# Kernel tuning notes

Hardware: AMD Instinct MI355X
Metric: run time of the kernel (lower is better)

The kernel has to match this reference:

```python
import jax, jax.numpy as jnp
import numpy as np

D_MODEL = 2048
EXPAND = 2
D_INNER = EXPAND * D_MODEL   # 4096
D_STATE = 128
D_CONV = 4
HEADDIM = 64
NHEADS = D_INNER // HEADDIM  # 64
NGROUPS = 1
CONV_DIM = D_INNER + 2 * NGROUPS * D_STATE           # 4352
D_IN_PROJ = 2 * D_INNER + 2 * NGROUPS * D_STATE + NHEADS  # 8512
B, T = 2, 2048
EPS = 1e-5


def setup_inputs() -> dict:
    key = jax.random.key(0)
    ks = jax.random.split(key, 12)
    x = jax.random.normal(ks[0], (B, T, D_MODEL), dtype=jnp.float32)
    cos = jax.random.normal(ks[1], (T, HEADDIM), dtype=jnp.float32)
    sin = jax.random.normal(ks[2], (T, HEADDIM), dtype=jnp.float32)
    in_proj_w = jax.random.normal(ks[3], (D_IN_PROJ, D_MODEL), dtype=jnp.float32) * 0.02
    conv_w = jax.random.normal(ks[4], (CONV_DIM, D_CONV), dtype=jnp.float32) * 0.2
    conv_b = jnp.zeros((CONV_DIM,), dtype=jnp.float32)
    # dt_bias = softplus^{-1}(dt) for dt ~ U[0.001, 0.1]
    dt = jax.random.uniform(ks[5], (NHEADS,), minval=0.001, maxval=0.1)
    dt_bias = (jnp.log(jnp.expm1(dt))).astype(jnp.float32)
    A_log = jnp.log(jax.random.uniform(ks[6], (NHEADS,), minval=1.0, maxval=16.0)).astype(jnp.float32)
    Dskip = jnp.ones((NHEADS,), dtype=jnp.float32)
    norm_w = jnp.ones((D_INNER,), dtype=jnp.float32)
    out_proj_w = jax.random.normal(ks[7], (D_MODEL, D_INNER), dtype=jnp.float32) * 0.02
    return {"x": x, "cos": cos, "sin": sin, "in_proj_w": in_proj_w,
            "conv_w": conv_w, "conv_b": conv_b, "dt_bias": dt_bias,
            "A_log": A_log, "Dskip": Dskip, "norm_w": norm_w,
            "out_proj_w": out_proj_w}


def _mamba2_fwd(x, in_proj_w, conv_w, conv_b, dt_bias, A_log, Dskip, norm_w, out_proj_w):
    # in_proj -> [z, xBC, dt]
    zxbcdt = jnp.einsum('btd,ed->bte', x, in_proj_w)  # [B,T,8512]
    z = zxbcdt[..., :D_INNER]
    xBC = zxbcdt[..., D_INNER:D_INNER + CONV_DIM]
    dt_raw = zxbcdt[..., D_INNER + CONV_DIM:]          # [B,T,H]

    # depthwise causal conv1d + SiLU
    xBC_pad = jnp.pad(xBC, ((0, 0), (D_CONV - 1, 0), (0, 0)))
    conv = conv_b
    for k in range(D_CONV):
        conv = conv + xBC_pad[:, k:k + T, :] * conv_w[:, k]
    xBC = jax.nn.silu(conv)

    x_ssm = xBC[..., :D_INNER].reshape(x.shape[0], T, NHEADS, HEADDIM)  # [B,T,H,P]
    Bmat = xBC[..., D_INNER:D_INNER + D_STATE]                          # [B,T,N] (ngroups=1)
    Cmat = xBC[..., D_INNER + D_STATE:]                                 # [B,T,N]

    dt = jax.nn.softplus(dt_raw + dt_bias)   # [B,T,H]
    A = -jnp.exp(A_log)                      # [H]
    dA = jnp.exp(dt * A)                     # [B,T,H], in (0,1]
    dtx = dt[..., None] * x_ssm              # [B,T,H,P]

    # selective scan over time (state h: [B,H,P,N])
    def step(h, xs_t):
        dA_t, dtx_t, B_t, C_t = xs_t  # [B,H],[B,H,P],[B,N],[B,N]
        h = h * dA_t[:, :, None, None] + dtx_t[:, :, :, None] * B_t[:, None, None, :]
        y = jnp.einsum('bhpn,bn->bhp', h, C_t)
        return h, y

    h0 = jnp.zeros((x.shape[0], NHEADS, HEADDIM, D_STATE), dtype=x.dtype)
    xs = (jnp.swapaxes(dA, 0, 1), jnp.swapaxes(dtx, 0, 1),
          jnp.swapaxes(Bmat, 0, 1), jnp.swapaxes(Cmat, 0, 1))
    _, ys = jax.lax.scan(step, h0, xs)       # ys: [T,B,H,P]
    y = jnp.swapaxes(ys, 0, 1) + Dskip[None, None, :, None] * x_ssm  # [B,T,H,P]
    y = y.reshape(x.shape[0], T, D_INNER)

    # gated RMSNorm: gate first, then normalize
    y = y * jax.nn.silu(z)
    y = y * jax.lax.rsqrt(jnp.mean(jnp.square(y), axis=-1, keepdims=True) + EPS) * norm_w

    return jnp.einsum('bte,de->btd', y, out_proj_w)  # [B,T,D]


def reference(x, cos, sin, in_proj_w, conv_w, conv_b, dt_bias, A_log, Dskip, norm_w, out_proj_w):
    # cos/sin accepted but ignored (Mamba needs no positional encoding)
    return _mamba2_fwd(x, in_proj_w, conv_w, conv_b, dt_bias, A_log, Dskip, norm_w, out_proj_w)
```

## Files before the change

kernel.cpp:

```cpp
#include <hip/hip_runtime.h>

#define D_MODEL 2048
#define D_INNER 4096
#define D_STATE 128
#define HEADDIM 64
#define NHEADS 64
#define CONV_DIM 4352
#define D_IN_PROJ 8512
#define BB 2
#define TSEQ 2048
#define BT (BB*TSEQ)
#define NCHUNK 32
#define LCH 64
#define EPS_F 1e-5f

typedef __bf16 bf16x8 __attribute__((ext_vector_type(8)));
typedef float f32x4 __attribute__((ext_vector_type(4)));

__device__ __forceinline__ float bf2f(unsigned short u){
  unsigned int x = ((unsigned int)u) << 16;
  return __builtin_bit_cast(float, x);
}
__device__ __forceinline__ unsigned short f2bf(float f){
  unsigned int x = __builtin_bit_cast(unsigned int, f);
  x += 0x7fffu + ((x >> 16) & 1u);
  return (unsigned short)(x >> 16);
}

__device__ __forceinline__ void async_copy16(const unsigned short* g, unsigned short* l) {
  __builtin_amdgcn_global_load_lds(
      (const __attribute__((address_space(1))) unsigned int*)g,
      (__attribute__((address_space(3))) unsigned int*)l, 16, 0, 0);
}

__global__ __launch_bounds__(256) void cast_kernel(
    const float* __restrict__ in, unsigned short* __restrict__ out, int n)
{
  int i = (blockIdx.x * 256 + threadIdx.x) * 8;
  if (i >= n) return;
  float4 a = *(const float4*)&in[i];
  float4 b = *(const float4*)&in[i + 4];
  unsigned short o[8] = { f2bf(a.x), f2bf(a.y), f2bf(a.z), f2bf(a.w),
                          f2bf(b.x), f2bf(b.y), f2bf(b.z), f2bf(b.w) };
  *(uint4*)&out[i] = *(uint4*)o;
}

template <bool F32OUT>
__global__ __launch_bounds__(256) void gemm_tn_kernel(
    const unsigned short* __restrict__ A, const unsigned short* __restrict__ Bm,
    void* __restrict__ Cout, int M, int N, int K, int NT, int MT)
{
  __shared__ __align__(16) unsigned short As[128 * 64];
  __shared__ __align__(16) unsigned short Bs[128 * 64];
  int tid = threadIdx.x;

  int bid = blockIdx.x;
  int fullBands = NT >> 3;
  int blocksFull = fullBands * 8 * MT;
  int mt, nt;
  if (bid < blocksFull) {
    int band = bid / (8 * MT);
    int wI = bid - band * (8 * MT);
    nt = band * 8 + (wI & 7);
    mt = wI >> 3;
  } else {
    int rem = bid - blocksFull;
    int WL = NT - fullBands * 8;
    nt = fullBands * 8 + rem % WL;
    mt = rem / WL;
  }
  int m0 = mt * 128, n0 = nt * 128;

  int wave = tid >> 6, lane = tid & 63;
  int wm = wave >> 1, wn = wave & 1;
  int lm = lane & 15, kqb = lane >> 4;
  int sw = lm & 7;

  int lr = lane >> 3, lc = lane & 7, bg = lc ^ lr;
  const unsigned short* Ap = A + (size_t)(m0 + wave * 32 + lr) * K + bg * 8;
  const unsigned short* Bp = Bm + (size_t)(n0 + wave * 32 + lr) * K + bg * 8;

  f32x4 acc[4][4] = {};

  for (int k0 = 0; k0 < K; k0 += 64) {
#pragma unroll
    for (int q = 0; q < 4; q++) {
      async_copy16(Ap + (size_t)q * 8 * K + k0, &As[(wave * 32 + q * 8) * 64]);
      async_copy16(Bp + (size_t)q * 8 * K + k0, &Bs[(wave * 32 + q * 8) * 64]);
    }
    __syncthreads();
#pragma unroll
    for (int kk = 0; kk < 64; kk += 32) {
      int b0 = (kk >> 3) + kqb;
      int boff = (b0 ^ sw) * 8;
      bf16x8 af[4], bfr[4];
#pragma unroll
      for (int i = 0; i < 4; i++) af[i]  = *(const bf16x8*)&As[(wm * 64 + i * 16 + lm) * 64 + boff];
#pragma unroll
      for (int j = 0; j < 4; j++) bfr[j] = *(const bf16x8*)&Bs[(wn * 64 + j * 16 + lm) * 64 + boff];
#pragma unroll
      for (int i = 0; i < 4; i++)
#pragma unroll
        for (int j = 0; j < 4; j++)
          acc[i][j] = __builtin_amdgcn_mfma_f32_16x16x32_bf16(af[i], bfr[j], acc[i][j], 0, 0, 0);
    }
    __syncthreads();
  }

  int rq = lane >> 4;
#pragma unroll
  for (int i = 0; i < 4; i++) {
#pragma unroll
    for (int j = 0; j < 4; j++) {
      int col = n0 + wn * 64 + j * 16 + lm;
      if (col < N) {
        int mrow = m0 + wm * 64 + i * 16 + rq * 4;
#pragma unroll
        for (int r = 0; r < 4; r++) {
          if (F32OUT) ((float*)Cout)[(size_t)(mrow + r) * N + col] = acc[i][j][r];
          else ((unsigned short*)Cout)[(size_t)(mrow + r) * N + col] = f2bf(acc[i][j][r]);
        }
      }
    }
  }
}

__global__ __launch_bounds__(256) void conv_silu_kernel(
    const unsigned short* __restrict__ zx, const float* __restrict__ conv_w,
    const float* __restrict__ conv_b, unsigned short* __restrict__ xconv,
    unsigned short* __restrict__ Bbf, unsigned short* __restrict__ Cbf)
{
  const int NG = CONV_DIM / 8;
  int gid = blockIdx.x * 256 + threadIdx.x;
  if (gid >= BT * NG) return;
  int cg = gid % NG; int bt = gid / NG;
  int t = bt % TSEQ;
  int c0 = cg * 8;

  float wgt[8][4];
#pragma unroll
  for (int i = 0; i < 8; i++)
#pragma unroll
    for (int k = 0; k < 4; k++) wgt[i][k] = conv_w[(c0 + i) * 4 + k];

  float acc[8];
#pragma unroll
  for (int i = 0; i < 8; i++) acc[i] = conv_b[c0 + i];

#pragma unroll
  for (int k = 0; k < 4; k++) {
    int ts = t - 3 + k;
    if (ts < 0) continue;
    unsigned short xv[8];
    *(uint4*)xv = *(const uint4*)&zx[(size_t)(bt - 3 + k) * D_IN_PROJ + D_INNER + c0];
#pragma unroll
    for (int i = 0; i < 8; i++) acc[i] = fmaf(bf2f(xv[i]), wgt[i][k], acc[i]);
  }

  unsigned short o[8];
#pragma unroll
  for (int i = 0; i < 8; i++) { float v = acc[i]; o[i] = f2bf(v / (1.f + expf(-v))); }
  if (c0 < D_INNER) {
    *(uint4*)&xconv[(size_t)bt * D_INNER + c0] = *(uint4*)o;
  } else if (c0 < D_INNER + D_STATE) {
    *(uint4*)&Bbf[(size_t)bt * D_STATE + (c0 - D_INNER)] = *(uint4*)o;
  } else {
    *(uint4*)&Cbf[(size_t)bt * D_STATE + (c0 - D_INNER - D_STATE)] = *(uint4*)o;
  }
}

__global__ __launch_bounds__(256) void dtcum_kernel(
    const unsigned short* __restrict__ zx, const float* __restrict__ dt_bias,
    const float* __restrict__ A_log, float* __restrict__ dtv, float* __restrict__ ca)
{
  int g = blockIdx.x * 4 + (threadIdx.x >> 6);
  int lane = threadIdx.x & 63;
  int h = g & 63; int cb = g >> 6;
  size_t bt = (size_t)cb * 64 + lane;
  float xr = bf2f(zx[bt * D_IN_PROJ + D_INNER + CONV_DIM + h]) + dt_bias[h];
  float dt = (xr > 20.f) ? xr : log1pf(expf(xr));
  float v = dt * (-expf(A_log[h]));
#pragma unroll
  for (int off = 1; off < 64; off <<= 1) {
    float t = __shfl_up(v, off);
    if (lane >= off) v += t;
  }
  dtv[bt * NHEADS + h] = dt;
  ca[(size_t)g * 64 + lane] = v;
}

__global__ __launch_bounds__(256) void chunk_g_kernel(
    const unsigned short* __restrict__ Bbf, const unsigned short* __restrict__ Cbf,
    unsigned short* __restrict__ G)
{
  __shared__ __align__(16) unsigned short Cs[64][136];
  __shared__ __align__(16) unsigned short Bs2[64][136];
  int tid = threadIdx.x; int cb = blockIdx.x;
  size_t bt0 = (size_t)cb * 64;
  int row = tid >> 2, seg = (tid & 3) * 32;
#pragma unroll
  for (int u = 0; u < 32; u += 8) {
    *(uint4*)&Cs[row][seg + u]  = *(const uint4*)&Cbf[(bt0 + row) * 128 + seg + u];
    *(uint4*)&Bs2[row][seg + u] = *(const uint4*)&Bbf[(bt0 + row) * 128 + seg + u];
  }
  __syncthreads();
  int wave = tid >> 6, lane = tid & 63, lm = lane & 15, kq = (lane >> 4) * 8, rq = lane >> 4;
  f32x4 acc[4] = {};
#pragma unroll
  for (int ks = 0; ks < 4; ks++) {
    bf16x8 af = *(const bf16x8*)&Cs[wave * 16 + lm][ks * 32 + kq];
#pragma unroll
    for (int jt = 0; jt < 4; jt++) {
      bf16x8 bb = *(const bf16x8*)&Bs2[jt * 16 + lm][ks * 32 + kq];
      acc[jt] = __builtin_amdgcn_mfma_f32_16x16x32_bf16(af, bb, acc[jt], 0, 0, 0);
    }
  }
#pragma unroll
  for (int jt = 0; jt < 4; jt++)
#pragma unroll
    for (int r = 0; r < 4; r++) {
      int i = wave * 16 + rq * 4 + r, j = jt * 16 + lm;
      G[(size_t)cb * 4096 + i * 64 + j] = f2bf(acc[jt][r]);
    }
}

__global__ __launch_bounds__(256) void chunk_state_kernel(
    const unsigned short* __restrict__ Bbf, const unsigned short* __restrict__ xconv,
    const float* __restrict__ dtv, const float* __restrict__ ca,
    unsigned short* __restrict__ S)
{
  __shared__ __align__(16) unsigned short Ax[64][72];
  __shared__ __align__(16) unsigned short Bn[128][72];
  int tid = threadIdx.x;
  int c = blockIdx.x & 31, hb = (blockIdx.x >> 5) & 15, b = blockIdx.x >> 9;
  int cb = b * 32 + c;
  size_t bt0 = (size_t)cb * 64;
  {
    int j = tid >> 2, nseg = (tid & 3) * 32;
    unsigned short bv[32];
#pragma unroll
    for (int u = 0; u < 32; u += 8)
      *(uint4*)&bv[u] = *(const uint4*)&Bbf[(bt0 + j) * 128 + nseg + u];
#pragma unroll
    for (int u = 0; u < 32; u++) Bn[nseg + u][j] = bv[u];
  }
  int wave = tid >> 6, lane = tid & 63, lm = lane & 15, kq = (lane >> 4) * 8, rq = lane >> 4;
  int j = tid >> 2, pseg = (tid & 3) * 16;
  for (int hh = 0; hh < 4; hh++) {
    int h = hb * 4 + hh;
    const float* cag = &ca[((size_t)cb * 64 + h) * 64];
    float wj = expf(cag[63] - cag[j]) * dtv[(bt0 + j) * 64 + h];
    unsigned short xv[16];
    *(uint4*)&xv[0] = *(const uint4*)&xconv[(bt0 + j) * 4096 + h * 64 + pseg];
    *(uint4*)&xv[8] = *(const uint4*)&xconv[(bt0 + j) * 4096 + h * 64 + pseg + 8];
    if (hh) __syncthreads();
#pragma unroll
    for (int q = 0; q < 16; q++) Ax[pseg + q][j] = f2bf(wj * bf2f(xv[q]));
    __syncthreads();
    f32x4 acc[8] = {};
#pragma unroll
    for (int ks = 0; ks < 2; ks++) {
      bf16x8 af = *(const bf16x8*)&Ax[wave * 16 + lm][ks * 32 + kq];
#pragma unroll
      for (int nt = 0; nt < 8; nt++) {
        bf16x8 bb = *(const bf16x8*)&Bn[nt * 16 + lm][ks * 32 + kq];
        acc[nt] = __builtin_amdgcn_mfma_f32_16x16x32_bf16(af, bb, acc[nt], 0, 0, 0);
      }
    }
    size_t sbase = ((size_t)(b * 64 + h) * 32 + c) * 8192;
#pragma unroll
    for (int nt = 0; nt < 8; nt++)
#pragma unroll
      for (int r = 0; r < 4; r++) {
        int p = wave * 16 + rq * 4 + r, n = nt * 16 + lm;
        S[sbase + p * 128 + n] = f2bf(acc[nt][r]);
      }
  }
}

__global__ __launch_bounds__(256) void state_pass_kernel(
    unsigned short* __restrict__ Shin, const float* __restrict__ ca)
{
  int part = blockIdx.x & 7, bh = blockIdx.x >> 3;
  int h = bh & 63, b = bh >> 6;
  int e0 = part * 1024 + threadIdx.x * 4;
  size_t base = (size_t)bh * 32 * 8192;
  float hc[4] = {0.f, 0.f, 0.f, 0.f};
  for (int c = 0; c < 32; c++) {
    float sc = expf(ca[(((size_t)(b * 32 + c)) * 64 + h) * 64 + 63]);
    size_t off = base + (size_t)c * 8192 + e0;
    uint2 sv = *(uint2*)&Shin[off];
    unsigned short* sp = (unsigned short*)&sv;
    unsigned short ho[4];
#pragma unroll
    for (int q = 0; q < 4; q++) ho[q] = f2bf(hc[q]);
    *(uint2*)&Shin[off] = *(uint2*)ho;
#pragma unroll
    for (int q = 0; q < 4; q++) hc[q] = sc * hc[q] + bf2f(sp[q]);
  }
}

__global__ __launch_bounds__(256) void chunk_y_kernel(
    const unsigned short* __restrict__ G, const unsigned short* __restrict__ Cbf,
    const unsigned short* __restrict__ xconv, const float* __restrict__ dtv,
    const float* __restrict__ ca, const unsigned short* __restrict__ hin,
    const float* __restrict__ Dskip, unsigned short* __restrict__ yp)
{
  __shared__ __align__(16) unsigned short Aop[64][200];
  __shared__ __align__(16) unsigned short Bop[64][200];
  __shared__ float cas[64]; __shared__ float dts[64];
  int tid = threadIdx.x;
  int c = blockIdx.x & 31, h = (blockIdx.x >> 5) & 63, b = blockIdx.x >> 11;
  int cb = b * 32 + c;
  size_t bt0 = (size_t)cb * 64;
  if (tid < 64) {
    cas[tid] = ca[((size_t)cb * 64 + h) * 64 + tid];
    dts[tid] = dtv[(bt0 + tid) * 64 + h];
  }
  __syncthreads();
  {
    int i = tid >> 2, jseg = (tid & 3) * 16;
    float cai = cas[i];
    unsigned short gv[16];
    *(uint4*)&gv[0] = *(const uint4*)&G[(size_t)cb * 4096 + i * 64 + jseg];
    *(uint4*)&gv[8] = *(const uint4*)&G[(size_t)cb * 4096 + i * 64 + jseg + 8];
    unsigned short o[16];
#pragma unroll
    for (int q = 0; q < 16; q++) {
      int j = jseg + q;
      float m = (j <= i) ? bf2f(gv[q]) * expf(cai - cas[j]) * dts[j] : 0.f;
      o[q] = f2bf(m);
    }
    *(uint4*)&Aop[i][jseg] = *(uint4*)&o[0];
    *(uint4*)&Aop[i][jseg + 8] = *(uint4*)&o[8];
  }
  {
    int i = tid >> 2, nseg = (tid & 3) * 32;
    float sci = expf(cas[i]);
#pragma unroll
    for (int u = 0; u < 32; u += 8) {
      unsigned short cv[8];
      *(uint4*)cv = *(const uint4*)&Cbf[(bt0 + i) * 128 + nseg + u];
      unsigned short o[8];
#pragma unroll
      for (int q = 0; q < 8; q++) o[q] = f2bf(sci * bf2f(cv[q]));
      *(uint4*)&Aop[i][64 + nseg + u] = *(uint4*)o;
    }
  }
  {
    int j = tid >> 2, pseg = (tid & 3) * 16;
    unsigned short xv[16];
    *(uint4*)&xv[0] = *(const uint4*)&xconv[(bt0 + j) * 4096 + h * 64 + pseg];
    *(uint4*)&xv[8] = *(const uint4*)&xconv[(bt0 + j) * 4096 + h * 64 + pseg + 8];
#pragma unroll
    for (int q = 0; q < 16; q++) Bop[pseg + q][j] = xv[q];
  }
  {
    int p = tid >> 2, nseg = (tid & 3) * 32;
    size_t hb = ((size_t)(b * 64 + h) * 32 + c) * 8192 + p * 128 + nseg;
#pragma unroll
    for (int u = 0; u < 32; u += 8)
      *(uint4*)&Bop[p][64 + nseg + u] = *(const uint4*)&hin[hb + u];
  }
  __syncthreads();
  int wave = tid >> 6, lane = tid & 63, lm = lane & 15, kq = (lane >> 4) * 8, rq = lane >> 4;
  f32x4 acc[4] = {};
#pragma unroll
  for (int ks = 0; ks < 6; ks++) {
    bf16x8 af = *(const bf16x8*)&Aop[wave * 16 + lm][ks * 32 + kq];
#pragma unroll
    for (int pt = 0; pt < 4; pt++) {
      bf16x8 bb = *(const bf16x8*)&Bop[pt * 16 + lm][ks * 32 + kq];
      acc[pt] = __builtin_amdgcn_mfma_f32_16x16x32_bf16(af, bb, acc[pt], 0, 0, 0);
    }
  }
  float dsk = Dskip[h];
#pragma unroll
  for (int pt = 0; pt < 4; pt++)
#pragma unroll
    for (int r = 0; r < 4; r++) {
      int i = wave * 16 + rq * 4 + r, p = pt * 16 + lm;
      float y = acc[pt][r] + dsk * bf2f(Bop[p][i]);
      yp[(bt0 + i) * 4096 + h * 64 + p] = f2bf(y);
    }
}

__global__ __launch_bounds__(256) void gate_norm_kernel(
    const unsigned short* __restrict__ yp, const unsigned short* __restrict__ zx,
    const float* __restrict__ norm_w, unsigned short* __restrict__ ybf)
{
  int row = blockIdx.x; int tid = threadIdx.x;
  int c0 = tid * 16;
  unsigned short y0[16], zv[16];
  const size_t base = (size_t)row * D_INNER + c0;
  *(uint4*)&y0[0] = *(const uint4*)&yp[base];
  *(uint4*)&y0[8] = *(const uint4*)&yp[base + 8];
  const size_t zbase = (size_t)row * D_IN_PROJ + c0;
  *(uint4*)&zv[0] = *(const uint4*)&zx[zbase];
  *(uint4*)&zv[8] = *(const uint4*)&zx[zbase + 8];

  float g[16]; float ss = 0.f;
#pragma unroll
  for (int i = 0; i < 16; i++) {
    float y = bf2f(y0[i]);
    float z = bf2f(zv[i]);
    float gate = z / (1.f + expf(-z));
    float gv = y * gate;
    g[i] = gv; ss += gv * gv;
  }
#pragma unroll
  for (int o = 32; o >= 1; o >>= 1) ss += __shfl_xor(ss, o);
  __shared__ float red[4]; __shared__ float stot;
  if ((tid & 63) == 0) red[tid >> 6] = ss;
  __syncthreads();
  if (tid == 0) stot = red[0] + red[1] + red[2] + red[3];
  __syncthreads();
  float scale = rsqrtf(stot * (1.f / D_INNER) + EPS_F);
  unsigned short o16[16];
#pragma unroll
  for (int i = 0; i < 16; i++) o16[i] = f2bf(g[i] * scale * norm_w[c0 + i]);
  *(uint4*)&ybf[base] = *(uint4*)&o16[0];
  *(uint4*)&ybf[base + 8] = *(uint4*)&o16[8];
}

extern "C" void kernel_launch(void* const* d_in, const int* in_sizes, int n_in,
                              void* d_out, int out_size, void* d_ws, size_t ws_size,
                              hipStream_t stream) {
  (void)in_sizes; (void)n_in; (void)out_size; (void)ws_size;
  const float* x          = (const float*)d_in[0];
  const float* in_proj_w  = (const float*)d_in[3];
  const float* conv_w     = (const float*)d_in[4];
  const float* conv_b     = (const float*)d_in[5];
  const float* dt_bias    = (const float*)d_in[6];
  const float* A_log      = (const float*)d_in[7];
  const float* Dskip      = (const float*)d_in[8];
  const float* norm_w     = (const float*)d_in[9];
  const float* out_proj_w = (const float*)d_in[10];
  float* out = (float*)d_out;

  char* w = (char*)d_ws;
  unsigned short* zx    = (unsigned short*)(w);
  unsigned short* xconv = (unsigned short*)(w + 69730304);
  unsigned short* Bbf = (unsigned short*)(w + 103284736);
  unsigned short* Cbf = (unsigned short*)(w + 105381888);
  float* dtv = (float*)(w + 107479040);
  float* ca  = (float*)(w + 109576192);
  unsigned short* G    = (unsigned short*)(w + 110624768);
  unsigned short* Shin = (unsigned short*)(w + 111149056);
  unsigned short* yp   = (unsigned short*)(w + 178257920);
  unsigned short* xb   = (unsigned short*)(w + 111149056);
  unsigned short* wib  = (unsigned short*)(w + 127926272);
  unsigned short* ybf  = (unsigned short*)(w + 111149056);
  unsigned short* wob  = (unsigned short*)(w + 144703488);

  cast_kernel<<<BT * D_MODEL / 8 / 256, 256, 0, stream>>>(x, xb, BT * D_MODEL);
  cast_kernel<<<D_IN_PROJ * D_MODEL / 8 / 256, 256, 0, stream>>>(in_proj_w, wib, D_IN_PROJ * D_MODEL);
  {
    int NT = (D_IN_PROJ + 127) / 128, MT = BT / 128;
    gemm_tn_kernel<false><<<NT * MT, 256, 0, stream>>>(
        xb, wib, zx, BT, D_IN_PROJ, D_MODEL, NT, MT);
  }
  conv_silu_kernel<<<(BT * (CONV_DIM / 8) + 255) / 256, 256, 0, stream>>>(
      zx, conv_w, conv_b, xconv, Bbf, Cbf);
  dtcum_kernel<<<BB * NCHUNK * NHEADS / 4, 256, 0, stream>>>(zx, dt_bias, A_log, dtv, ca);
  chunk_g_kernel<<<BB * NCHUNK, 256, 0, stream>>>(Bbf, Cbf, G);
  chunk_state_kernel<<<BB * 16 * NCHUNK, 256, 0, stream>>>(Bbf, xconv, dtv, ca, Shin);
  state_pass_kernel<<<BB * NHEADS * 8, 256, 0, stream>>>(Shin, ca);
  chunk_y_kernel<<<BB * NHEADS * NCHUNK, 256, 0, stream>>>(G, Cbf, xconv, dtv, ca, Shin, Dskip, yp);
  gate_norm_kernel<<<BT, 256, 0, stream>>>(yp, zx, norm_w, ybf);
  cast_kernel<<<D_MODEL * D_INNER / 8 / 256, 256, 0, stream>>>(out_proj_w, wob, D_MODEL * D_INNER);
  {
    int NT = D_MODEL / 128, MT = BT / 128;
    gemm_tn_kernel<true><<<NT * MT, 256, 0, stream>>>(
        ybf, wob, out, BT, D_MODEL, D_INNER, NT, MT);
  }
}
```

Measured before the change: 599.5 us.

## Add 256x256-tile multi-stage pipelined GEMM for input projection

Adds a new bf16 MFMA GEMM kernel for the input projection. It uses 256x256 output tiles, 512 threads, a 4-deep LDS ring buffer of 32-wide K slices, split A/B async prefetch and raised wave priority around the MFMA blocks. The larger tile raises data reuse per loaded byte, and the deeper pipeline is meant to hide global load latency better than the 128x128 single-buffer kernel. In exchange it uses more registers and LDS per block. The last N tile also reads weight rows past the end of the matrix, relying on workspace slack, with stores guarded.

```diff
diff --git a/kernel.cpp b/kernel.cpp
--- a/kernel.cpp
+++ b/kernel.cpp
@@ -46,12 +46,12 @@
 }
 
 template <bool F32OUT>
-__global__ __launch_bounds__(256) void gemm_tn_kernel(
+__global__ __launch_bounds__(512, 2) void gemm256_kernel(
     const unsigned short* __restrict__ A, const unsigned short* __restrict__ Bm,
     void* __restrict__ Cout, int M, int N, int K, int NT, int MT)
 {
-  __shared__ __align__(16) unsigned short As[128 * 64];
-  __shared__ __align__(16) unsigned short Bs[128 * 64];
+  __shared__ __align__(16) unsigned short As[4][256 * 32];
+  __shared__ __align__(16) unsigned short Bs[4][256 * 32];
   int tid = threadIdx.x;
 
   int bid = blockIdx.x;
@@ -69,6 +69,118 @@
     nt = fullBands * 8 + rem % WL;
     mt = rem / WL;
   }
+  int m0 = mt * 256, n0 = nt * 256;
+
+  int wid = tid >> 6, lane = tid & 63;
+  int wm = wid >> 2, wn = wid & 3;
+  int lm = lane & 15, kqb = lane >> 4;
+  int rsw = (kqb ^ (lm & 3)) * 8;
+
+  int srow = tid >> 2;
+  int sblk = (tid & 3) ^ (srow & 3);
+  const unsigned short* Ap = A + (size_t)(m0 + srow) * K + sblk * 8;
+  const unsigned short* Bp = Bm + (size_t)(n0 + srow) * K + sblk * 8;
+
+  f32x4 acc[8][4] = {};
+  const int U = K >> 5;
+
+#pragma unroll
+  for (int u = 0; u < 3; u++) {
+    int ku = u << 5;
+    async_copy16(Ap + ku, &As[u][wid * 512]);
+    async_copy16(Ap + (size_t)128 * K + ku, &As[u][4096 + wid * 512]);
+    async_copy16(Bp + ku, &Bs[u][wid * 512]);
+    async_copy16(Bp + (size_t)128 * K + ku, &Bs[u][4096 + wid * 512]);
+  }
+
+  for (int u = 0; u < U; u++) {
+    int s = u & 3;
+    int left = U - 1 - u;
+    if (left >= 2)      asm volatile("s_waitcnt vmcnt(8)" ::: "memory");
+    else if (left == 1) asm volatile("s_waitcnt vmcnt(4)" ::: "memory");
+    else                asm volatile("s_waitcnt vmcnt(0)" ::: "memory");
+    __builtin_amdgcn_s_barrier();
+
+    const unsigned short* Ab = &As[s][wm * 4096];
+    const unsigned short* Bb = &Bs[s][(wn * 64) * 32];
+    int up = u + 3;
+    int kup = up << 5, sp = up & 3;
+
+    bf16x8 bfr[4], af[4];
+#pragma unroll
+    for (int j = 0; j < 4; j++) bfr[j] = *(const bf16x8*)&Bb[(j * 16 + lm) * 32 + rsw];
+#pragma unroll
+    for (int i = 0; i < 4; i++) af[i] = *(const bf16x8*)&Ab[(i * 16 + lm) * 32 + rsw];
+    if (up < U) {
+      async_copy16(Ap + kup, &As[sp][wid * 512]);
+      async_copy16(Ap + (size_t)128 * K + kup, &As[sp][4096 + wid * 512]);
+    }
+    __builtin_amdgcn_s_setprio(1);
+#pragma unroll
+    for (int i = 0; i < 4; i++)
+#pragma unroll
+      for (int j = 0; j < 4; j++)
+        acc[i][j] = __builtin_amdgcn_mfma_f32_16x16x32_bf16(af[i], bfr[j], acc[i][j], 0, 0, 0);
+    __builtin_amdgcn_s_setprio(0);
+    __builtin_amdgcn_s_barrier();
+
+#pragma unroll
+    for (int i = 0; i < 4; i++) af[i] = *(const bf16x8*)&Ab[((4 + i) * 16 + lm) * 32 + rsw];
+    if (up < U) {
+      async_copy16(Bp + kup, &Bs[sp][wid * 512]);
+      async_copy16(Bp + (size_t)128 * K + kup, &Bs[sp][4096 + wid * 512]);
+    }
+    __builtin_amdgcn_s_setprio(1);
+#pragma unroll
+    for (int i = 0; i < 4; i++)
+#pragma unroll
+      for (int j = 0; j < 4; j++)
+        acc[4 + i][j] = __builtin_amdgcn_mfma_f32_16x16x32_bf16(af[i], bfr[j], acc[4 + i][j], 0, 0, 0);
+    __builtin_amdgcn_s_setprio(0);
+  }
+
+  int rq = lane >> 4;
+#pragma unroll
+  for (int i = 0; i < 8; i++) {
+#pragma unroll
+    for (int j = 0; j < 4; j++) {
+      int col = n0 + wn * 64 + j * 16 + lm;
+      if (col < N) {
+        int mrow = m0 + wm * 128 + i * 16 + rq * 4;
+#pragma unroll
+        for (int r = 0; r < 4; r++) {
+          if (F32OUT) ((float*)Cout)[(size_t)(mrow + r) * N + col] = acc[i][j][r];
+          else ((unsigned short*)Cout)[(size_t)(mrow + r) * N + col] = f2bf(acc[i][j][r]);
+        }
+      }
+    }
+  }
+}
+
+template <bool F32OUT>
+__global__ __launch_bounds__(256) void gemm_tn_kernel(
+    const unsigned short* __restrict__ A, const unsigned short* __restrict__ Bm,
+    void* __restrict__ Cout, int M, int N, int K, int NT, int MT)
+{
+  __shared__ __align__(16) unsigned short As[128 * 64];
+  __shared__ __align__(16) unsigned short Bs[128 * 64];
+  int tid = threadIdx.x;
+
+  int bid = blockIdx.x;
+  int fullBands = NT >> 3;
+  int blocksFull = fullBands * 8 * MT;
+  int mt, nt;
+  if (bid < blocksFull) {
+    int band = bid / (8 * MT);
+    int wI = bid - band * (8 * MT);
+    nt = band * 8 + (wI & 7);
+    mt = wI >> 3;
+  } else {
+    int rem = bid - blocksFull;
+    int WL = NT - fullBands * 8;
+    nt = fullBands * 8 + rem % WL;
+    mt = rem / WL;
+  }
   int m0 = mt * 128, n0 = nt * 128;
 
   int wave = tid >> 6, lane = tid & 63;
@@ -456,8 +568,8 @@
   cast_kernel<<<BT * D_MODEL / 8 / 256, 256, 0, stream>>>(x, xb, BT * D_MODEL);
   cast_kernel<<<D_IN_PROJ * D_MODEL / 8 / 256, 256, 0, stream>>>(in_proj_w, wib, D_IN_PROJ * D_MODEL);
   {
-    int NT = (D_IN_PROJ + 127) / 128, MT = BT / 128;
-    gemm_tn_kernel<false><<<NT * MT, 256, 0, stream>>>(
+    int NT = 34, MT = BT / 256;
+    gemm256_kernel<false><<<NT * MT, 512, 0, stream>>>(
         xb, wib, zx, BT, D_IN_PROJ, D_MODEL, NT, MT);
   }
   conv_silu_kernel<<<(BT * (CONV_DIM / 8) + 255) / 256, 256, 0, stream>>>(
```

Measured after the change: 614.5 us. 1.02x slower.

## Add 256x256 double-buffered, software-pipelined GEMM kernel for the input projection

Applied to the files above, without the earlier changes.

Adds a new GEMM kernel with 512 threads and 256x256 output tiles. It double-buffers A and B in LDS and interleaves async global-to-LDS loads with MFMA quarters, using explicit vmcnt waits, barriers and s_setprio. The kernel is used only for the in_proj GEMM, replacing the 128x128 single-buffered kernel. It aims to raise data reuse per tile and overlap loads with compute. In exchange it uses much more LDS per block and creates a partial last N tile whose B loads read past the weight rows; output stores are guarded.

```diff
diff --git a/kernel.cpp b/kernel.cpp
--- a/kernel.cpp
+++ b/kernel.cpp
@@ -45,13 +45,79 @@
   *(uint4*)&out[i] = *(uint4*)o;
 }
 
+#define LDA8(s_, row_, b0_) \
+  (*(const bf16x8*)&As[s_][((row_) << 6) + ((((b0_) ^ sw) << 3))])
+#define LDB8(s_, row_, b0_) \
+  (*(const bf16x8*)&Bs[s_][((row_) << 6) + ((((b0_) ^ sw) << 3))])
+
+#define RDQ(DST, s_, q_)                                                      \
+  _Pragma("unroll") for (int rf_ = 0; rf_ < 2; rf_++)                         \
+  _Pragma("unroll") for (int k_ = 0; k_ < 2; k_++)                            \
+    DST[rf_*2+k_] = LDA8(s_, wm*128 + (q_)*32 + rf_*16 + lm, 4*k_ + kqb);
+
+#define RDBF(DST, s_)                                                         \
+  _Pragma("unroll") for (int cf_ = 0; cf_ < 4; cf_++)                         \
+  _Pragma("unroll") for (int k_ = 0; k_ < 2; k_++)                            \
+    DST[cf_*2+k_] = LDB8(s_, wn*64 + cf_*16 + lm, 4*k_ + kqb);
+
+#define MFMAQ(q_, AF, BF)                                                     \
+  __builtin_amdgcn_s_setprio(1);                                              \
+  _Pragma("unroll") for (int rf_ = 0; rf_ < 2; rf_++)                         \
+  _Pragma("unroll") for (int cf_ = 0; cf_ < 4; cf_++)                         \
+  _Pragma("unroll") for (int k_ = 0; k_ < 2; k_++)                            \
+    acc[(q_)*2+rf_][cf_] = __builtin_amdgcn_mfma_f32_16x16x32_bf16(           \
+        AF[rf_*2+k_], BF[cf_*2+k_], acc[(q_)*2+rf_][cf_], 0, 0, 0);           \
+  __builtin_amdgcn_s_setprio(0);
+
+#define SA(t_, h_)                                                            \
+  _Pragma("unroll") for (int i_ = 0; i_ < 2; i_++)                            \
+    async_copy16(ApS + ((size_t)((h_)*128 + i_*8))*K + (size_t)(t_)*64,       \
+                 &As[(t_)&1][((h_)*128 + wid*16 + i_*8) * 64]);
+
+#define SB(t_, h_)                                                            \
+  _Pragma("unroll") for (int i_ = 0; i_ < 2; i_++)                            \
+    async_copy16(BpS + ((size_t)((h_)*128 + i_*8))*K + (size_t)(t_)*64,       \
+                 &Bs[(t_)&1][((h_)*128 + wid*16 + i_*8) * 64]);
+
+#define GTILE(t_, BC, BN)                                                     \
+  {                                                                           \
+    const int s_ = (t_) & 1;                                                  \
+                                                                      \
+    RDQ(aN, s_, 1);                                                           \
+    if ((t_) + 1 < U) SA((t_) + 1, 1);                                        \
+    if ((t_) + 2 < U) SB((t_) + 2, 0);                                        \
+    MFMAQ(0, aC, BC);                                                         \
+    __builtin_amdgcn_s_barrier();                                             \
+                                                                      \
+    RDQ(aC, s_, 2);                                                           \
+    if ((t_) + 2 < U) SB((t_) + 2, 1);                                        \
+    MFMAQ(1, aN, BC);                                                         \
+    __builtin_amdgcn_s_barrier();                                             \
+                                                                      \
+    RDQ(aN, s_, 3);                                                           \
+    MFMAQ(2, aC, BC);                                                         \
+    __builtin_amdgcn_s_barrier();                                             \
+                                                       \
+    if ((t_) + 1 < U) {                                                       \
+      if ((t_) + 3 <= U) { asm volatile("s_waitcnt vmcnt(4)" ::: "memory"); } \
+      else               { asm volatile("s_waitcnt vmcnt(0)" ::: "memory"); } \
+      __builtin_amdgcn_s_barrier();                                           \
+      __builtin_amdgcn_sched_barrier(0);                                      \
+      if ((t_) + 2 < U) SA((t_) + 2, 0);                                      \
+      RDQ(aC, s_ ^ 1, 0);                                                     \
+      RDBF(BN, s_ ^ 1);                                                       \
+    }                                                                         \
+    MFMAQ(3, aN, BC);                                                         \
+    __builtin_amdgcn_s_barrier();                                             \
+  }
+
 template <bool F32OUT>
-__global__ __launch_bounds__(256) void gemm_tn_kernel(
+__global__ __launch_bounds__(512, 2) void gemm256_kernel(
     const unsigned short* __restrict__ A, const unsigned short* __restrict__ Bm,
     void* __restrict__ Cout, int M, int N, int K, int NT, int MT)
 {
-  __shared__ __align__(16) unsigned short As[128 * 64];
-  __shared__ __align__(16) unsigned short Bs[128 * 64];
+  __shared__ __align__(16) unsigned short As[2][256 * 64];
+  __shared__ __align__(16) unsigned short Bs[2][256 * 64];
   int tid = threadIdx.x;
 
   int bid = blockIdx.x;
@@ -69,6 +135,77 @@
     nt = fullBands * 8 + rem % WL;
     mt = rem / WL;
   }
+  int m0 = mt * 256, n0 = nt * 256;
+
+  int wid = tid >> 6, lane = tid & 63;
+  int wm = wid >> 2, wn = wid & 3;
+  int lm = lane & 15, kqb = lane >> 4;
+  int sw = lm & 7;
+
+  int sblk = (lane & 7) ^ (lane >> 3);
+  const unsigned short* ApS = A + (size_t)(m0 + wid * 16 + (lane >> 3)) * K + sblk * 8;
+  const unsigned short* BpS = Bm + (size_t)(n0 + wid * 16 + (lane >> 3)) * K + sblk * 8;
+
+  f32x4 acc[8][4] = {};
+  const int U = K >> 6;
+
+  SA(0, 0); SA(0, 1); SB(0, 0); SB(0, 1);
+  SA(1, 0); SB(1, 0); SB(1, 1);
+  asm volatile("s_waitcnt vmcnt(6)" ::: "memory");
+  __builtin_amdgcn_s_barrier();
+  __builtin_amdgcn_sched_barrier(0);
+
+  bf16x8 aC[4], aN[4], bC[8], bN[8];
+  RDBF(bC, 0);
+  RDQ(aC, 0, 0);
+
+  for (int t = 0; t < U; t += 2) {
+    GTILE(t,     bC, bN);
+    GTILE(t + 1, bN, bC);
+  }
+
+  int rq = lane >> 4;
+#pragma unroll
+  for (int i = 0; i < 8; i++) {
+#pragma unroll
+    for (int j = 0; j < 4; j++) {
+      int col = n0 + wn * 64 + j * 16 + lm;
+      if (col < N) {
+        int mrow = m0 + wm * 128 + i * 16 + rq * 4;
+#pragma unroll
+        for (int r = 0; r < 4; r++) {
+          if (F32OUT) ((float*)Cout)[(size_t)(mrow + r) * N + col] = acc[i][j][r];
+          else ((unsigned short*)Cout)[(size_t)(mrow + r) * N + col] = f2bf(acc[i][j][r]);
+        }
+      }
+    }
+  }
+}
+
+template <bool F32OUT>
+__global__ __launch_bounds__(256) void gemm_tn_kernel(
+    const unsigned short* __restrict__ A, const unsigned short* __restrict__ Bm,
+    void* __restrict__ Cout, int M, int N, int K, int NT, int MT)
+{
+  __shared__ __align__(16) unsigned short As[128 * 64];
+  __shared__ __align__(16) unsigned short Bs[128 * 64];
+  int tid = threadIdx.x;
+
+  int bid = blockIdx.x;
+  int fullBands = NT >> 3;
+  int blocksFull = fullBands * 8 * MT;
+  int mt, nt;
+  if (bid < blocksFull) {
+    int band = bid / (8 * MT);
+    int wI = bid - band * (8 * MT);
+    nt = band * 8 + (wI & 7);
+    mt = wI >> 3;
+  } else {
+    int rem = bid - blocksFull;
+    int WL = NT - fullBands * 8;
+    nt = fullBands * 8 + rem % WL;
+    mt = rem / WL;
+  }
   int m0 = mt * 128, n0 = nt * 128;
 
   int wave = tid >> 6, lane = tid & 63;
@@ -456,8 +593,8 @@
   cast_kernel<<<BT * D_MODEL / 8 / 256, 256, 0, stream>>>(x, xb, BT * D_MODEL);
   cast_kernel<<<D_IN_PROJ * D_MODEL / 8 / 256, 256, 0, stream>>>(in_proj_w, wib, D_IN_PROJ * D_MODEL);
   {
-    int NT = (D_IN_PROJ + 127) / 128, MT = BT / 128;
-    gemm_tn_kernel<false><<<NT * MT, 256, 0, stream>>>(
+    int NT = 34, MT = BT / 256;
+    gemm256_kernel<false><<<NT * MT, 512, 0, stream>>>(
         xb, wib, zx, BT, D_IN_PROJ, D_MODEL, NT, MT);
   }
   conv_silu_kernel<<<(BT * (CONV_DIM / 8) + 255) / 256, 256, 0, stream>>>(
```

Measured after the change: 627.4 us. 4.6% more time.
